# Performance work log

Measured on AMD Instinct MI355X. Metric: run time of the kernel, lower is better.

The kernel has to match this reference:

```python
import jax, jax.numpy as jnp
import numpy as np

B, S_SPARSE, N_NUM, VOCAB = 512, 7, 6, 100
D, H, DFF, L = 1024, 16, 4096, 4
DH = D // 2  # 512, numeric encoding width
HD = D // H  # head dim 64
EPS = 1e-5


def setup_inputs() -> dict:
    key = jax.random.key(0)
    ks = jax.random.split(key, 16)
    inp = {
        'sparse': jax.random.randint(ks[0], (B, S_SPARSE), 0, VOCAB, dtype=jnp.int64),
        'numeric': jax.random.randint(ks[1], (B, N_NUM), 0, 100000, dtype=jnp.int32),
        'sparse_emb': jax.random.normal(ks[2], (VOCAB, D), jnp.float32),
        'numeric_emb': jax.random.normal(ks[3], (N_NUM, DH), jnp.float32),
        'Wqkv': jax.random.normal(ks[4], (L, 3 * D, D), jnp.float32) * 0.02,
        'bqkv': jnp.zeros((L, 3 * D), jnp.float32),
        'Wo': jax.random.normal(ks[5], (L, D, D), jnp.float32) * 0.02,
        'bo': jnp.zeros((L, D), jnp.float32),
        'W1': jax.random.normal(ks[6], (L, DFF, D), jnp.float32) * 0.02,
        'b1': jnp.zeros((L, DFF), jnp.float32),
        'W2': jax.random.normal(ks[7], (L, D, DFF), jnp.float32) * 0.02,
        'b2': jnp.zeros((L, D), jnp.float32),
        'ln1_g': jnp.ones((L, D), jnp.float32), 'ln1_b': jnp.zeros((L, D), jnp.float32),
        'ln2_g': jnp.ones((L, D), jnp.float32), 'ln2_b': jnp.zeros((L, D), jnp.float32),
    }
    return inp


def _ln(x, g, b):
    m = jnp.mean(x, -1, keepdims=True)
    v = jnp.mean((x - m) ** 2, -1, keepdims=True)
    return (x - m) * jax.lax.rsqrt(v + EPS) * g + b


def _encode_numeric(numeric):
    # piecewise-linear (thermometer) encoding, vectorized over batch & features
    mins = jnp.zeros((N_NUM,), jnp.float32)
    maxs = jnp.array([DH, DH, 100000.0, 100000.0, 100000.0, 100000.0], jnp.float32)
    scaled = (numeric.astype(jnp.float32) - mins) / (maxs - mins) * DH  # [B, 6]
    return jnp.clip(scaled[..., None] - jnp.arange(DH, dtype=jnp.float32), 0.0, 1.0)  # [B,6,DH]


def reference(sparse, numeric, sparse_emb, numeric_emb, Wqkv, bqkv, Wo, bo,
              W1, b1, W2, b2, ln1_g, ln1_b, ln2_g, ln2_b):
    enc = _encode_numeric(numeric)  # [B,6,DH]
    num_tok = jnp.concatenate(
        [enc, jnp.broadcast_to(numeric_emb[None], (sparse.shape[0], N_NUM, DH))], axis=2)  # [B,6,D]
    x = jnp.concatenate([sparse_emb[sparse], num_tok], axis=1)  # [B,13,D]

    scale = 1.0 / np.sqrt(HD)
    for l in range(L):
        qkv = jnp.einsum('bsd,ed->bse', x, Wqkv[l]) + bqkv[l]
        q, k, v = jnp.split(qkv, 3, axis=-1)
        bsz, s = x.shape[0], x.shape[1]
        q = q.reshape(bsz, s, H, HD)
        k = k.reshape(bsz, s, H, HD)
        v = v.reshape(bsz, s, H, HD)
        attn = jax.nn.softmax(jnp.einsum('bqhd,bkhd->bhqk', q, k) * scale, axis=-1)
        o = jnp.einsum('bhqk,bkhd->bqhd', attn, v).reshape(bsz, s, D)
        o = jnp.einsum('bsd,ed->bse', o, Wo[l]) + bo[l]
        x = _ln(x + o, ln1_g[l], ln1_b[l])  # post-norm
        h = jax.nn.gelu(jnp.einsum('bsd,fd->bsf', x, W1[l]) + b1[l], approximate=False)
        ff = jnp.einsum('bsf,df->bsd', h, W2[l]) + b2[l]
        x = _ln(x + ff, ln2_g[l], ln2_b[l])
    return x
```

## Files before the change

kernel.cpp:

```cpp
#include <hip/hip_runtime.h>
#include <hip/hip_bf16.h>
#include <cstdint>
#include <cmath>


typedef __bf16 bf16x8 __attribute__((ext_vector_type(8)));
typedef float  f32x4  __attribute__((ext_vector_type(4)));

__device__ __forceinline__ void async16(void* lds, const void* g) {
  __builtin_amdgcn_global_load_lds(
      (const __attribute__((address_space(1))) unsigned int*)g,
      (__attribute__((address_space(3))) unsigned int*)lds, 16, 0, 0);
}

__global__ __launch_bounds__(256) void f2b_kernel(const float* __restrict__ s,
                                                  __bf16* __restrict__ d, int n8) {
  int i = blockIdx.x * 256 + threadIdx.x;
  if (i >= n8) return;
  const float4* s4 = (const float4*)s;
  float4 a = s4[2 * i], b = s4[2 * i + 1];
  bf16x8 o;
  o[0] = (__bf16)a.x; o[1] = (__bf16)a.y; o[2] = (__bf16)a.z; o[3] = (__bf16)a.w;
  o[4] = (__bf16)b.x; o[5] = (__bf16)b.y; o[6] = (__bf16)b.z; o[7] = (__bf16)b.w;
  *(bf16x8*)(d + (size_t)i * 8) = o;
}

__global__ __launch_bounds__(256) void build_x_kernel(
    const int* __restrict__ sparse, const int* __restrict__ numeric,
    const float* __restrict__ semb, const float* __restrict__ nemb,
    float* __restrict__ xf, __bf16* __restrict__ xb) {
  int r = blockIdx.x;
  int b = r / 13, s = r % 13;
  int t = threadIdx.x;
  size_t base = (size_t)r * 1024;
  if (s < 7) {
    int tok = sparse[b * 7 + s];
    const float* src = semb + (size_t)tok * 1024;
    for (int d = t; d < 1024; d += 256) {
      float v = src[d];
      xf[base + d] = v; xb[base + d] = (__bf16)v;
    }
  } else {
    int j = s - 7;
    float nv = (float)numeric[b * 6 + j];
    float scaled = nv * (j < 2 ? 1.0f : 512.0f / 100000.0f);
    for (int d = t; d < 1024; d += 256) {
      float v;
      if (d < 512) v = fminf(fmaxf(scaled - (float)d, 0.0f), 1.0f);
      else         v = nemb[j * 512 + (d - 512)];
      xf[base + d] = v; xb[base + d] = (__bf16)v;
    }
  }
}

template <int EPI>
__global__ __launch_bounds__(256) void gemm_bt(
    const __bf16* __restrict__ A, const __bf16* __restrict__ Bw,
    const float* __restrict__ bias, float* __restrict__ Cf,
    __bf16* __restrict__ Cb, int N, int K) {
  __shared__ __attribute__((aligned(16))) __bf16 As[128 * 32];
  __shared__ __attribute__((aligned(16))) __bf16 Bs[128 * 32];
  const int t = threadIdx.x;
  const int bm = blockIdx.x, bn = blockIdx.y;
  const int lane = t & 63, wid = t >> 6;
  const int wm = (wid >> 1) << 6, wn = (wid & 1) << 6;
  const int lm = lane & 15, lq = lane >> 4;
  const int arow = t >> 2, acol = (t & 3) << 3;
  const __bf16* Ag = A + (size_t)(bm * 128 + arow) * K + acol;
  const __bf16* Bg = Bw + (size_t)(bn * 128 + arow) * K + acol;
  const size_t half = (size_t)64 * K;
  const __bf16* a_rd = As + (wm + lm) * 32 + lq * 8;
  const __bf16* b_rd = Bs + (wn + lm) * 32 + lq * 8;
  f32x4 acc[4][4] = {};
  for (int k0 = 0; k0 < K; k0 += 32) {
    __syncthreads();
    async16(As + t * 8,        Ag);
    async16(As + 2048 + t * 8, Ag + half);
    async16(Bs + t * 8,        Bg);
    async16(Bs + 2048 + t * 8, Bg + half);
    Ag += 32; Bg += 32;
    asm volatile("s_waitcnt vmcnt(0)" ::: "memory");
    __syncthreads();
    bf16x8 af[4], bf[4];
#pragma unroll
    for (int i = 0; i < 4; i++) af[i] = *(const bf16x8*)(a_rd + i * 16 * 32);
#pragma unroll
    for (int i = 0; i < 4; i++) bf[i] = *(const bf16x8*)(b_rd + i * 16 * 32);
#pragma unroll
    for (int mi = 0; mi < 4; mi++)
#pragma unroll
      for (int ni = 0; ni < 4; ni++)
        acc[mi][ni] = __builtin_amdgcn_mfma_f32_16x16x32_bf16(af[mi], bf[ni], acc[mi][ni], 0, 0, 0);
  }
  const int row0 = bm * 128 + wm + lq * 4;
  const int col0 = bn * 128 + wn + lm;
#pragma unroll
  for (int mi = 0; mi < 4; mi++) {
#pragma unroll
    for (int ni = 0; ni < 4; ni++) {
      int col = col0 + ni * 16;
      float bv = bias[col];
#pragma unroll
      for (int r = 0; r < 4; r++) {
        int row = row0 + mi * 16 + r;
        float v = acc[mi][ni][r] + bv;
        if (EPI == 2) v = v * 0.5f * (1.0f + erff(v * 0.70710678118f));
        if (EPI == 0) Cf[(size_t)row * N + col] = v;
        else          Cb[(size_t)row * N + col] = (__bf16)v;
      }
    }
  }
}

__global__ __launch_bounds__(64) void attn_kernel(const __bf16* __restrict__ qkv,
                                                  __bf16* __restrict__ o) {
  int bh = blockIdx.x;
  int b = bh >> 4, h = bh & 15;
  int lane = threadIdx.x;
  __shared__ float qs[13][68], ks[13][68], vs[13][68];
  __shared__ float S[13][16];
  const __bf16* base = qkv + (size_t)b * 13 * 3072 + h * 64 + lane;
#pragma unroll
  for (int i = 0; i < 13; i++) {
    qs[i][lane] = (float)base[(size_t)i * 3072];
    ks[i][lane] = (float)base[(size_t)i * 3072 + 1024];
    vs[i][lane] = (float)base[(size_t)i * 3072 + 2048];
  }
  __syncthreads();
  for (int rep = 0; rep < 3; rep++) {
    int idx = lane + rep * 64;
    if (idx < 169) {
      int i = idx / 13, j = idx % 13;
      float s = 0.f;
#pragma unroll
      for (int d = 0; d < 64; d++) s += qs[i][d] * ks[j][d];
      S[i][j] = s * 0.125f;
    }
  }
  __syncthreads();
  if (lane < 13) {
    float m = S[lane][0];
#pragma unroll
    for (int j = 1; j < 13; j++) m = fmaxf(m, S[lane][j]);
    float sum = 0.f;
#pragma unroll
    for (int j = 0; j < 13; j++) { float e = expf(S[lane][j] - m); S[lane][j] = e; sum += e; }
    float inv = 1.0f / sum;
#pragma unroll
    for (int j = 0; j < 13; j++) S[lane][j] *= inv;
  }
  __syncthreads();
  __bf16* ob = o + (size_t)b * 13 * 1024 + h * 64 + lane;
#pragma unroll
  for (int i = 0; i < 13; i++) {
    float s = 0.f;
#pragma unroll
    for (int j = 0; j < 13; j++) s += S[i][j] * vs[j][lane];
    ob[(size_t)i * 1024] = (__bf16)s;
  }
}

__global__ __launch_bounds__(256) void add_ln_kernel(
    const float* __restrict__ xin, const float* __restrict__ delta,
    const float* __restrict__ g, const float* __restrict__ bta,
    float* __restrict__ xf_out, __bf16* __restrict__ xb_out) {
  int r = blockIdx.x, t = threadIdx.x;
  size_t base = (size_t)r * 1024;
  float vals[4], s = 0.f, s2 = 0.f;
#pragma unroll
  for (int i = 0; i < 4; i++) {
    int d = t + i * 256;
    float v = xin[base + d] + delta[base + d];
    vals[i] = v; s += v; s2 += v * v;
  }
  __shared__ float red[8];
  for (int off = 32; off > 0; off >>= 1) { s += __shfl_down(s, off); s2 += __shfl_down(s2, off); }
  if ((t & 63) == 0) { red[t >> 6] = s; red[4 + (t >> 6)] = s2; }
  __syncthreads();
  float S1 = red[0] + red[1] + red[2] + red[3];
  float S2 = red[4] + red[5] + red[6] + red[7];
  float mean = S1 * (1.0f / 1024.0f);
  float var  = S2 * (1.0f / 1024.0f) - mean * mean;
  float inv  = rsqrtf(var + 1e-5f);
#pragma unroll
  for (int i = 0; i < 4; i++) {
    int d = t + i * 256;
    float y = (vals[i] - mean) * inv * g[d] + bta[d];
    xf_out[base + d] = y;
    xb_out[base + d] = (__bf16)y;
  }
}

extern "C" void kernel_launch(void* const* d_in, const int* in_sizes, int n_in,
                              void* d_out, int out_size, void* d_ws, size_t ws_size,
                              hipStream_t stream) {
  const int*   sparse  = (const int*)d_in[0];
  const int*   numeric = (const int*)d_in[1];
  const float* semb    = (const float*)d_in[2];
  const float* nemb    = (const float*)d_in[3];
  const float* Wqkv    = (const float*)d_in[4];
  const float* bqkv    = (const float*)d_in[5];
  const float* Wo      = (const float*)d_in[6];
  const float* bo      = (const float*)d_in[7];
  const float* W1      = (const float*)d_in[8];
  const float* b1      = (const float*)d_in[9];
  const float* W2      = (const float*)d_in[10];
  const float* b2      = (const float*)d_in[11];
  const float* ln1g    = (const float*)d_in[12];
  const float* ln1b    = (const float*)d_in[13];
  const float* ln2g    = (const float*)d_in[14];
  const float* ln2b    = (const float*)d_in[15];
  float* out = (float*)d_out;

  char* ws = (char*)d_ws;
  size_t off = 0;
  auto carve = [&](size_t bytes) -> char* {
    char* p = ws + off; off += (bytes + 255) & ~(size_t)255; return p;
  };
  __bf16* wb   = (__bf16*)carve((size_t)4096 * 1024 * 2);
  float*  xf   = (float*) carve((size_t)6656 * 1024 * 4);
  __bf16* xb   = (__bf16*)carve((size_t)6656 * 1024 * 2);
  char*   pool = carve((size_t)6656 * 4096 * 2);
  __bf16* qkvb  = (__bf16*)pool;
  __bf16* attnb = (__bf16*)(pool + (size_t)6656 * 3072 * 2);
  __bf16* hb    = (__bf16*)pool;
  float*  tmpf  = out;

  build_x_kernel<<<6656, 256, 0, stream>>>(sparse, numeric, semb, nemb, xf, xb);

  for (int l = 0; l < 4; ++l) {
    f2b_kernel<<<1536, 256, 0, stream>>>(Wqkv + (size_t)l * 3145728, wb, 393216);
    gemm_bt<1><<<dim3(52, 24), 256, 0, stream>>>(xb, wb, bqkv + l * 3072, nullptr, qkvb, 3072, 1024);
    attn_kernel<<<8192, 64, 0, stream>>>(qkvb, attnb);
    f2b_kernel<<<512, 256, 0, stream>>>(Wo + (size_t)l * 1048576, wb, 131072);
    gemm_bt<0><<<dim3(52, 8), 256, 0, stream>>>(attnb, wb, bo + l * 1024, tmpf, nullptr, 1024, 1024);
    add_ln_kernel<<<6656, 256, 0, stream>>>(xf, tmpf, ln1g + l * 1024, ln1b + l * 1024, xf, xb);
    f2b_kernel<<<2048, 256, 0, stream>>>(W1 + (size_t)l * 4194304, wb, 524288);
    gemm_bt<2><<<dim3(52, 32), 256, 0, stream>>>(xb, wb, b1 + l * 4096, nullptr, hb, 4096, 1024);
    f2b_kernel<<<2048, 256, 0, stream>>>(W2 + (size_t)l * 4194304, wb, 524288);
    gemm_bt<0><<<dim3(52, 8), 256, 0, stream>>>(hb, wb, b2 + l * 1024, tmpf, nullptr, 1024, 4096);
    float* xdst = (l == 3) ? out : xf;
    add_ln_kernel<<<6656, 256, 0, stream>>>(xf, tmpf, ln2g + l * 1024, ln2b + l * 1024, xdst, xb);
  }
}
```

Baseline: 1.622 ms.

## Use BK=64 swizzled LDS tiles, tanh-approx GELU, and merge Wqkv/Wo conversions

The GEMM K-tile grows from 32 to 64 and LDS rows use an XOR swizzle, which halves the number of barriers per K and avoids bank conflicts on fragment reads. The exact erf GELU is replaced with a tanh approximation built from exp and a fast reciprocal, which lowers epilogue cost but changes the numerics relative to the exact-GELU reference. The Wqkv and Wo fp32-to-bf16 conversions are merged into one launch, saving a kernel launch per layer. The larger tiles double LDS use per block, which may lower occupancy.

After: 1.439 ms. 1.13x faster.

```diff
diff --git a/kernel.cpp b/kernel.cpp
--- a/kernel.cpp
+++ b/kernel.cpp
@@ -23,6 +23,21 @@
   o[0] = (__bf16)a.x; o[1] = (__bf16)a.y; o[2] = (__bf16)a.z; o[3] = (__bf16)a.w;
   o[4] = (__bf16)b.x; o[5] = (__bf16)b.y; o[6] = (__bf16)b.z; o[7] = (__bf16)b.w;
   *(bf16x8*)(d + (size_t)i * 8) = o;
+}
+
+__global__ __launch_bounds__(256) void f2b2_kernel(
+    const float* __restrict__ s0, __bf16* __restrict__ d0, int n0,
+    const float* __restrict__ s1, __bf16* __restrict__ d1, int n8) {
+  int i = blockIdx.x * 256 + threadIdx.x;
+  if (i >= n8) return;
+  const float* s; __bf16* d; int j;
+  if (i < n0) { s = s0; d = d0; j = i; } else { s = s1; d = d1; j = i - n0; }
+  const float4* s4 = (const float4*)s;
+  float4 a = s4[2 * j], b = s4[2 * j + 1];
+  bf16x8 o;
+  o[0] = (__bf16)a.x; o[1] = (__bf16)a.y; o[2] = (__bf16)a.z; o[3] = (__bf16)a.w;
+  o[4] = (__bf16)b.x; o[5] = (__bf16)b.y; o[6] = (__bf16)b.z; o[7] = (__bf16)b.w;
+  *(bf16x8*)(d + (size_t)j * 8) = o;
 }
 
 __global__ __launch_bounds__(256) void build_x_kernel(
@@ -58,39 +73,51 @@
     const __bf16* __restrict__ A, const __bf16* __restrict__ Bw,
     const float* __restrict__ bias, float* __restrict__ Cf,
     __bf16* __restrict__ Cb, int N, int K) {
-  __shared__ __attribute__((aligned(16))) __bf16 As[128 * 32];
-  __shared__ __attribute__((aligned(16))) __bf16 Bs[128 * 32];
+  __shared__ __attribute__((aligned(16))) __bf16 As[128 * 64];
+  __shared__ __attribute__((aligned(16))) __bf16 Bs[128 * 64];
   const int t = threadIdx.x;
   const int bm = blockIdx.x, bn = blockIdx.y;
   const int lane = t & 63, wid = t >> 6;
   const int wm = (wid >> 1) << 6, wn = (wid & 1) << 6;
   const int lm = lane & 15, lq = lane >> 4;
-  const int arow = t >> 2, acol = (t & 3) << 3;
-  const __bf16* Ag = A + (size_t)(bm * 128 + arow) * K + acol;
-  const __bf16* Bg = Bw + (size_t)(bn * 128 + arow) * K + acol;
-  const size_t half = (size_t)64 * K;
-  const __bf16* a_rd = As + (wm + lm) * 32 + lq * 8;
-  const __bf16* b_rd = Bs + (wn + lm) * 32 + lq * 8;
+  const int srow = t >> 3, sp = t & 7;
+  const int sc = sp ^ (srow & 7);
+  const __bf16* Ag = A + (size_t)(bm * 128 + srow) * K + sc * 8;
+  const __bf16* Bg = Bw + (size_t)(bn * 128 + srow) * K + sc * 8;
+  const size_t rstep = (size_t)32 * K;
   f32x4 acc[4][4] = {};
-  for (int k0 = 0; k0 < K; k0 += 32) {
+  const int nIter = K >> 6;
+  for (int k0 = 0; k0 < nIter; ++k0) {
     __syncthreads();
-    async16(As + t * 8,        Ag);
-    async16(As + 2048 + t * 8, Ag + half);
-    async16(Bs + t * 8,        Bg);
-    async16(Bs + 2048 + t * 8, Bg + half);
-    Ag += 32; Bg += 32;
+#pragma unroll
+    for (int r = 0; r < 4; ++r) {
+      async16(As + r * 2048 + t * 8, Ag + r * rstep);
+      async16(Bs + r * 2048 + t * 8, Bg + r * rstep);
+    }
+    Ag += 64; Bg += 64;
     asm volatile("s_waitcnt vmcnt(0)" ::: "memory");
     __syncthreads();
-    bf16x8 af[4], bf[4];
-#pragma unroll
-    for (int i = 0; i < 4; i++) af[i] = *(const bf16x8*)(a_rd + i * 16 * 32);
-#pragma unroll
-    for (int i = 0; i < 4; i++) bf[i] = *(const bf16x8*)(b_rd + i * 16 * 32);
-#pragma unroll
-    for (int mi = 0; mi < 4; mi++)
-#pragma unroll
-      for (int ni = 0; ni < 4; ni++)
-        acc[mi][ni] = __builtin_amdgcn_mfma_f32_16x16x32_bf16(af[mi], bf[ni], acc[mi][ni], 0, 0, 0);
+#pragma unroll
+    for (int kk = 0; kk < 2; ++kk) {
+      bf16x8 af[4], bf[4];
+#pragma unroll
+      for (int i = 0; i < 4; i++) {
+        int row = wm + i * 16 + lm;
+        int pc = ((kk << 2) + lq) ^ (lm & 7);
+        af[i] = *(const bf16x8*)(As + row * 64 + pc * 8);
+      }
+#pragma unroll
+      for (int i = 0; i < 4; i++) {
+        int row = wn + i * 16 + lm;
+        int pc = ((kk << 2) + lq) ^ (lm & 7);
+        bf[i] = *(const bf16x8*)(Bs + row * 64 + pc * 8);
+      }
+#pragma unroll
+      for (int mi = 0; mi < 4; mi++)
+#pragma unroll
+        for (int ni = 0; ni < 4; ni++)
+          acc[mi][ni] = __builtin_amdgcn_mfma_f32_16x16x32_bf16(af[mi], bf[ni], acc[mi][ni], 0, 0, 0);
+    }
   }
   const int row0 = bm * 128 + wm + lq * 4;
   const int col0 = bn * 128 + wn + lm;
@@ -104,7 +131,13 @@
       for (int r = 0; r < 4; r++) {
         int row = row0 + mi * 16 + r;
         float v = acc[mi][ni][r] + bv;
-        if (EPI == 2) v = v * 0.5f * (1.0f + erff(v * 0.70710678118f));
+        if (EPI == 2) {
+          float u = fabsf(v);
+          float y = 0.7978845608f * u * (1.0f + 0.044715f * u * u);
+          float e = __expf(-2.0f * y);
+          float th = (1.0f - e) * __builtin_amdgcn_rcpf(1.0f + e);
+          v = 0.5f * v * (1.0f + (v < 0.0f ? -th : th));
+        }
         if (EPI == 0) Cf[(size_t)row * N + col] = v;
         else          Cb[(size_t)row * N + col] = (__bf16)v;
       }
@@ -229,11 +262,11 @@
   build_x_kernel<<<6656, 256, 0, stream>>>(sparse, numeric, semb, nemb, xf, xb);
 
   for (int l = 0; l < 4; ++l) {
-    f2b_kernel<<<1536, 256, 0, stream>>>(Wqkv + (size_t)l * 3145728, wb, 393216);
+    f2b2_kernel<<<2048, 256, 0, stream>>>(Wqkv + (size_t)l * 3145728, wb, 393216,
+                                          Wo + (size_t)l * 1048576, wb + 3145728, 524288);
     gemm_bt<1><<<dim3(52, 24), 256, 0, stream>>>(xb, wb, bqkv + l * 3072, nullptr, qkvb, 3072, 1024);
     attn_kernel<<<8192, 64, 0, stream>>>(qkvb, attnb);
-    f2b_kernel<<<512, 256, 0, stream>>>(Wo + (size_t)l * 1048576, wb, 131072);
-    gemm_bt<0><<<dim3(52, 8), 256, 0, stream>>>(attnb, wb, bo + l * 1024, tmpf, nullptr, 1024, 1024);
+    gemm_bt<0><<<dim3(52, 8), 256, 0, stream>>>(attnb, wb + 3145728, bo + l * 1024, tmpf, nullptr, 1024, 1024);
     add_ln_kernel<<<6656, 256, 0, stream>>>(xf, tmpf, ln1g + l * 1024, ln1b + l * 1024, xf, xb);
     f2b_kernel<<<2048, 256, 0, stream>>>(W1 + (size_t)l * 4194304, wb, 524288);
     gemm_bt<2><<<dim3(52, 32), 256, 0, stream>>>(xb, wb, b1 + l * 4096, nullptr, hb, 4096, 1024);
```
